# Performance work log

Measured on AMD Instinct MI355X. Metric: run time of the kernel, lower is better.

Reference implementation:

```python
import jax, jax.numpy as jnp
import numpy as np

D_MODEL = 1024
NUM_HEADS = 16
D_FF = 4096
BATCH = 4
SEQ = 1024
EPS = 1e-5
ROPE_THETA = 10000.0


def trunc_normal(key, shape):
    # approximate torch trunc_normal_(mean=0, std=1, a=-2, b=2)
    return jax.random.truncated_normal(key, -2.0, 2.0, shape, dtype=jnp.float32)


def setup_inputs() -> dict:
    key = jax.random.key(0)
    ks = jax.random.split(key, 10)
    d, h, f = D_MODEL, NUM_HEADS, D_FF
    return {
        "x": jax.random.normal(ks[0], (BATCH, SEQ, d), dtype=jnp.float32),
        "wq": trunc_normal(ks[1], (d, d)),
        "wk": trunc_normal(ks[2], (d, d)),
        "wv": trunc_normal(ks[3], (d, d)),
        "wo": trunc_normal(ks[4], (d, d)),
        "w1": trunc_normal(ks[5], (f, d)),
        "w2": trunc_normal(ks[6], (d, f)),
        "w3": trunc_normal(ks[7], (f, d)),
        "g1": trunc_normal(ks[8], (d,)),
        "g2": trunc_normal(ks[9], (d,)),
    }


def rms_norm(x, g):
    # source sums (x^2 + eps) then divides by d -> mean(x^2) + eps
    rms = jnp.sqrt(jnp.mean(jnp.square(x), axis=-1, keepdims=True) + EPS)
    return x * g / rms


def apply_rope(x, pos):
    # x: [b, h, s, d_k]; interleaved-pair rotation, theta=ROPE_THETA
    dk = x.shape[-1]
    inv_freq = ROPE_THETA ** (-jnp.arange(0, dk, 2, dtype=jnp.float32) / dk)
    ang = pos[:, None].astype(jnp.float32) * inv_freq[None, :]  # [s, dk/2]
    cos, sin = jnp.cos(ang), jnp.sin(ang)
    x1, x2 = x[..., 0::2], x[..., 1::2]
    r1 = x1 * cos - x2 * sin
    r2 = x1 * sin + x2 * cos
    return jnp.stack([r1, r2], axis=-1).reshape(x.shape)


def reference(x, wq, wk, wv, wo, w1, w2, w3, g1, g2):
    b, s, d = x.shape
    h, dk = NUM_HEADS, d // NUM_HEADS
    pos = jnp.arange(s)

    # --- attention sub-block (pre-norm) ---
    y = rms_norm(x, g1)
    q = (y @ wq.T).reshape(b, s, h, dk).transpose(0, 2, 1, 3)
    k = (y @ wk.T).reshape(b, s, h, dk).transpose(0, 2, 1, 3)
    v = (y @ wv.T).reshape(b, s, h, dk).transpose(0, 2, 1, 3)
    q = apply_rope(q, pos)
    k = apply_rope(k, pos)
    scores = jnp.einsum('bhqd,bhkd->bhqk', q, k) / jnp.sqrt(jnp.float32(dk))
    causal = jnp.tril(jnp.ones((s, s), dtype=bool))
    scores = jnp.where(causal, scores, -jnp.inf)
    attn = jax.nn.softmax(scores, axis=-1)
    ctx = jnp.einsum('bhqk,bhkd->bhqd', attn, v)
    ctx = ctx.transpose(0, 2, 1, 3).reshape(b, s, d)
    x = x + ctx @ wo.T

    # --- SwiGLU FFN sub-block (pre-norm) ---
    y = rms_norm(x, g2)
    l1 = y @ w1.T
    glu = (jax.nn.sigmoid(l1) * l1) * (y @ w3.T)
    return x + glu @ w2.T
```

## Files before the change

### kernel.cpp

```cpp
#include <hip/hip_runtime.h>

typedef __bf16 bf16;
typedef __attribute__((ext_vector_type(8))) __bf16 bf16x8;
typedef __attribute__((ext_vector_type(4))) float f32x4;

static __device__ __forceinline__ int swz4(int r) { return (r & 3) ^ ((r >> 2) & 3); }

static __device__ __forceinline__ void async_cp16(void* lds, const void* g) {
  __builtin_amdgcn_global_load_lds((__attribute__((address_space(1))) void*)g,
                                   (__attribute__((address_space(3))) void*)lds,
                                   16, 0, 0);
}

static __device__ __forceinline__ f32x4 mfma16(bf16x8 a, bf16x8 b, f32x4 c) {
  return __builtin_amdgcn_mfma_f32_16x16x32_bf16(a, b, c, 0, 0, 0);
}

static __device__ __forceinline__ unsigned short bfbits(float f) {
  bf16 b = (bf16)f;
  return __builtin_bit_cast(unsigned short, b);
}

extern "C" __global__ void prep_kernel(
    const float* __restrict__ wq, const float* __restrict__ wk,
    const float* __restrict__ wv, const float* __restrict__ wo,
    const float* __restrict__ w1, const float* __restrict__ w3,
    const float* __restrict__ w2,
    unsigned short* __restrict__ WQH, unsigned short* __restrict__ WQL,
    unsigned short* __restrict__ WKH, unsigned short* __restrict__ WKL,
    unsigned short* __restrict__ WVH, unsigned short* __restrict__ WOH,
    unsigned short* __restrict__ W1H, unsigned short* __restrict__ W3H,
    unsigned short* __restrict__ W2H, float2* __restrict__ rope) {
  const int seg = blockIdx.y;
  const int i = blockIdx.x * 256 + threadIdx.x;
  if (seg == 7) {
    if (i >= 32768) return;
    int s = i >> 5, fi = i & 31;
    float inv_freq = powf(10000.0f, -(2.0f * (float)fi) / 64.0f);
    float ang = (float)s * inv_freq;
    float2 cs;
    cs.x = cosf(ang);
    cs.y = sinf(ang);
    rope[i] = cs;
    return;
  }
  const float* src;
  unsigned short* hi_;
  unsigned short* lo_ = nullptr;
  int n4;
  switch (seg) {
    case 0: src = wq; hi_ = WQH; lo_ = WQL; n4 = 262144; break;
    case 1: src = wk; hi_ = WKH; lo_ = WKL; n4 = 262144; break;
    case 2: src = wv; hi_ = WVH; n4 = 262144; break;
    case 3: src = wo; hi_ = WOH; n4 = 262144; break;
    case 4: src = w1; hi_ = W1H; n4 = 1048576; break;
    case 5: src = w3; hi_ = W3H; n4 = 1048576; break;
    default: src = w2; hi_ = W2H; n4 = 1048576; break;
  }
  if (i >= n4) return;
  float4 v = ((const float4*)src)[i];
  bf16 b0 = (bf16)v.x, b1 = (bf16)v.y, b2 = (bf16)v.z, b3 = (bf16)v.w;
  ushort4 oh;
  oh.x = __builtin_bit_cast(unsigned short, b0);
  oh.y = __builtin_bit_cast(unsigned short, b1);
  oh.z = __builtin_bit_cast(unsigned short, b2);
  oh.w = __builtin_bit_cast(unsigned short, b3);
  ((ushort4*)hi_)[i] = oh;
  if (lo_) {
    ushort4 ol;
    ol.x = bfbits(v.x - (float)b0);
    ol.y = bfbits(v.y - (float)b1);
    ol.z = bfbits(v.z - (float)b2);
    ol.w = bfbits(v.w - (float)b3);
    ((ushort4*)lo_)[i] = ol;
  }
}

extern "C" __global__ __launch_bounds__(256) void rmsnorm_kernel(
    const float* __restrict__ x, const float* __restrict__ g,
    unsigned short* __restrict__ yhi, unsigned short* __restrict__ ylo) {
  int row = blockIdx.x;
  int t = threadIdx.x;
  const float4 xv = *(const float4*)(x + (size_t)row * 1024 + t * 4);
  float ss = xv.x * xv.x + xv.y * xv.y + xv.z * xv.z + xv.w * xv.w;
#pragma unroll
  for (int d = 1; d < 64; d <<= 1) ss += __shfl_xor(ss, d, 64);
  __shared__ float red[4];
  if ((t & 63) == 0) red[t >> 6] = ss;
  __syncthreads();
  float tot = red[0] + red[1] + red[2] + red[3];
  float inv = 1.0f / sqrtf(tot * (1.0f / 1024.0f) + 1e-5f);
  const float4 gv = *(const float4*)(g + t * 4);
  float y0 = xv.x * gv.x * inv, y1 = xv.y * gv.y * inv;
  float y2 = xv.z * gv.z * inv, y3 = xv.w * gv.w * inv;
  bf16 b0 = (bf16)y0, b1 = (bf16)y1, b2 = (bf16)y2, b3 = (bf16)y3;
  ushort4 oh;
  oh.x = __builtin_bit_cast(unsigned short, b0);
  oh.y = __builtin_bit_cast(unsigned short, b1);
  oh.z = __builtin_bit_cast(unsigned short, b2);
  oh.w = __builtin_bit_cast(unsigned short, b3);
  ((ushort4*)yhi)[(size_t)row * 256 + t] = oh;
  if (ylo) {
    ushort4 ol;
    ol.x = bfbits(y0 - (float)b0);
    ol.y = bfbits(y1 - (float)b1);
    ol.z = bfbits(y2 - (float)b2);
    ol.w = bfbits(y3 - (float)b3);
    ((ushort4*)ylo)[(size_t)row * 256 + t] = ol;
  }
}

template <int EPI>
__global__ __launch_bounds__(256, 2) void gemm_nt(
    const bf16* __restrict__ A, const bf16* __restrict__ B, int M, int N, int K, int ldk,
    float* __restrict__ outF, bf16* __restrict__ outB,
    const float* __restrict__ resF) {
  A += (size_t)blockIdx.z * K;
  B += (size_t)blockIdx.z * K;
  __shared__ alignas(16) bf16 As[128 * 32];
  __shared__ alignas(16) bf16 Bs[128 * 32];
  const int tid = threadIdx.x;
  const int lane = tid & 63, wave = tid >> 6;
  const int lo = lane & 15, hi = lane >> 4;
  const int wm = wave >> 1, wn = wave & 1;
  const size_t tm = (size_t)blockIdx.y * 128, tn = (size_t)blockIdx.x * 128;
  f32x4 acc[4][4] = {};
  for (int k0 = 0; k0 < K; k0 += 32) {
    __syncthreads();
#pragma unroll
    for (int i2 = 0; i2 < 2; i2++) {
      int p = tid + 256 * i2;
      int row = p >> 2, kcp = p & 3;
      int kcl = kcp ^ swz4(row);
      async_cp16((char*)As + (size_t)p * 16, A + (tm + row) * (size_t)ldk + k0 + kcl * 8);
      async_cp16((char*)Bs + (size_t)p * 16, B + (tn + row) * (size_t)ldk + k0 + kcl * 8);
    }
    __syncthreads();
    bf16x8 fa[4], fb[4];
#pragma unroll
    for (int i = 0; i < 4; i++) {
      int ra = wm * 64 + i * 16 + lo;
      fa[i] = *(const bf16x8*)((const char*)As + ra * 64 + ((hi ^ swz4(ra)) << 4));
      int rb = wn * 64 + i * 16 + lo;
      fb[i] = *(const bf16x8*)((const char*)Bs + rb * 64 + ((hi ^ swz4(rb)) << 4));
    }
    __builtin_amdgcn_s_setprio(1);
#pragma unroll
    for (int i = 0; i < 4; i++)
#pragma unroll
      for (int j = 0; j < 4; j++) acc[i][j] = mfma16(fa[i], fb[j], acc[i][j]);
    __builtin_amdgcn_s_setprio(0);
  }
#pragma unroll
  for (int i = 0; i < 4; i++)
#pragma unroll
    for (int j = 0; j < 4; j++)
#pragma unroll
      for (int r = 0; r < 4; r++) {
        size_t m = tm + wm * 64 + i * 16 + hi * 4 + r;
        size_t n = tn + wn * 64 + j * 16 + lo;
        float v = acc[i][j][r];
        if constexpr (EPI == 0) {
          size_t idx = (((m >> 10) * 16 + (n >> 6)) * 64 + (n & 63)) * 1024 + (m & 1023);
          outB[idx] = (bf16)v;
        } else if constexpr (EPI == 1) {
          size_t idx = m * (size_t)N + n;
          outF[idx] = v + resF[idx];
        } else {
          atomicAdd(&outF[m * (size_t)N + n], v);
        }
      }
}

extern "C" __global__ __launch_bounds__(512, 2) void gemm_up_kernel(
    const bf16* __restrict__ A, const bf16* __restrict__ B1,
    const bf16* __restrict__ B3, bf16* __restrict__ G) {
  __shared__ alignas(16) bf16 LA[2][2][256][32];
  __shared__ alignas(16) bf16 LB1[2][2][128][32];
  __shared__ alignas(16) bf16 LB3[2][2][128][32];
  const int tid = threadIdx.x;
  const int lane = tid & 63, wave = tid >> 6;
  const int lo = lane & 15, hi = lane >> 4;
  const int wm = wave >> 1, wn = wave & 1;
  const size_t tm = (size_t)blockIdx.y * 256, tn = (size_t)blockIdx.x * 128;

  f32x4 acc1[4][4] = {}, acc3[4][4] = {};

  auto stageA = [&](int kt, int kh, int buf) {
#pragma unroll
    for (int i2 = 0; i2 < 2; i2++) {
      int s = i2 * 512 + tid;
      int r = s >> 2, c = s & 3;
      async_cp16((char*)&LA[buf][kh][0][0] + (size_t)s * 16,
                 A + (tm + r) * (size_t)1024 + kt * 64 + kh * 32 + ((c ^ (r & 3)) << 3));
    }
  };
  auto stageB = [&](const bf16* __restrict__ Bsrc, bf16* dstBase, int kt, int kh) {
    int r = tid >> 2, c = tid & 3;
    async_cp16((char*)dstBase + (size_t)tid * 16,
               Bsrc + (tn + r) * (size_t)1024 + kt * 64 + kh * 32 + ((c ^ (r & 3)) << 3));
  };

  stageA(0, 0, 0);
  stageB(B1, &LB1[0][0][0][0], 0, 0);
  stageB(B3, &LB3[0][0][0][0], 0, 0);
  stageA(0, 1, 0);
  stageB(B1, &LB1[0][1][0][0], 0, 1);
  stageB(B3, &LB3[0][1][0][0], 0, 1);
  stageA(1, 0, 1);
  stageB(B1, &LB1[1][0][0][0], 1, 0);
  stageB(B3, &LB3[1][0][0][0], 1, 0);
  asm volatile("s_waitcnt vmcnt(4)");
  __builtin_amdgcn_s_barrier();

  for (int t = 0; t < 16; t++) {
    const int p = t & 1;
    bf16x8 fa[4], fb[4];
#pragma unroll
    for (int i = 0; i < 4; i++) {
      int ra = wm * 64 + i * 16 + lo;
      fa[i] = *(const bf16x8*)&LA[p][0][ra][(hi ^ (ra & 3)) << 3];
      int rb = wn * 64 + i * 16 + lo;
      fb[i] = *(const bf16x8*)&LB1[p][0][rb][(hi ^ (rb & 3)) << 3];
    }
    if (t + 1 < 16) stageA(t + 1, 1, p ^ 1);
    __builtin_amdgcn_s_barrier();
    asm volatile("s_waitcnt lgkmcnt(0)");
    __builtin_amdgcn_sched_barrier(0);
    __builtin_amdgcn_s_setprio(1);
#pragma unroll
    for (int i = 0; i < 4; i++)
#pragma unroll
      for (int j = 0; j < 4; j++) acc1[i][j] = mfma16(fa[i], fb[j], acc1[i][j]);
    __builtin_amdgcn_s_setprio(0);
    __builtin_amdgcn_s_barrier();
#pragma unroll
    for (int i = 0; i < 4; i++) {
      int rb = wn * 64 + i * 16 + lo;
      fb[i] = *(const bf16x8*)&LB3[p][0][rb][(hi ^ (rb & 3)) << 3];
    }
    if (t + 1 < 16) {
      stageB(B1, &LB1[p ^ 1][1][0][0], t + 1, 1);
      stageB(B3, &LB3[p ^ 1][1][0][0], t + 1, 1);
    }
    __builtin_amdgcn_s_barrier();
    asm volatile("s_waitcnt lgkmcnt(0)");
    __builtin_amdgcn_sched_barrier(0);
    __builtin_amdgcn_s_setprio(1);
#pragma unroll
    for (int i = 0; i < 4; i++)
#pragma unroll
      for (int j = 0; j < 4; j++) acc3[i][j] = mfma16(fa[i], fb[j], acc3[i][j]);
    __builtin_amdgcn_s_setprio(0);
    __builtin_amdgcn_s_barrier();
#pragma unroll
    for (int i = 0; i < 4; i++) {
      int ra = wm * 64 + i * 16 + lo;
      fa[i] = *(const bf16x8*)&LA[p][1][ra][(hi ^ (ra & 3)) << 3];
      int rb = wn * 64 + i * 16 + lo;
      fb[i] = *(const bf16x8*)&LB1[p][1][rb][(hi ^ (rb & 3)) << 3];
    }
    if (t + 2 < 16) stageA(t + 2, 0, p);
    __builtin_amdgcn_s_barrier();
    asm volatile("s_waitcnt lgkmcnt(0)");
    __builtin_amdgcn_sched_barrier(0);
    __builtin_amdgcn_s_setprio(1);
#pragma unroll
    for (int i = 0; i < 4; i++)
#pragma unroll
      for (int j = 0; j < 4; j++) acc1[i][j] = mfma16(fa[i], fb[j], acc1[i][j]);
    __builtin_amdgcn_s_setprio(0);
    __builtin_amdgcn_s_barrier();
#pragma unroll
    for (int i = 0; i < 4; i++) {
      int rb = wn * 64 + i * 16 + lo;
      fb[i] = *(const bf16x8*)&LB3[p][1][rb][(hi ^ (rb & 3)) << 3];
    }
    if (t + 2 < 16) {
      stageB(B1, &LB1[p][0][0][0], t + 2, 0);
      stageB(B3, &LB3[p][0][0][0], t + 2, 0);
    }
    __builtin_amdgcn_s_barrier();
    asm volatile("s_waitcnt lgkmcnt(0)");
    __builtin_amdgcn_sched_barrier(0);
    __builtin_amdgcn_s_setprio(1);
#pragma unroll
    for (int i = 0; i < 4; i++)
#pragma unroll
      for (int j = 0; j < 4; j++) acc3[i][j] = mfma16(fa[i], fb[j], acc3[i][j]);
    __builtin_amdgcn_s_setprio(0);
    if (t + 2 < 16) {
      asm volatile("s_waitcnt vmcnt(4)");
    } else if (t + 1 < 16) {
      asm volatile("s_waitcnt vmcnt(0)");
    }
    __builtin_amdgcn_s_barrier();
  }

#pragma unroll
  for (int i = 0; i < 4; i++)
#pragma unroll
    for (int j = 0; j < 4; j++)
#pragma unroll
      for (int r = 0; r < 4; r++) {
        size_t m = tm + wm * 64 + i * 16 + hi * 4 + r;
        size_t n = tn + wn * 64 + j * 16 + lo;
        float v1 = acc1[i][j][r], v3 = acc3[i][j][r];
        G[m * 4096 + n] = (bf16)(v1 / (1.0f + __expf(-v1)) * v3);
      }
}

extern "C" __global__ __launch_bounds__(256, 2) void gemm_qk_kernel(
    const bf16* __restrict__ Ah, const bf16* __restrict__ Al,
    const bf16* __restrict__ BhQ, const bf16* __restrict__ BlQ,
    const bf16* __restrict__ BhK, const bf16* __restrict__ BlK,
    const float2* __restrict__ rope,
    bf16* __restrict__ OhQ, bf16* __restrict__ OlQ,
    bf16* __restrict__ OhK, bf16* __restrict__ OlK) {
  const bf16* Bh = blockIdx.z ? BhK : BhQ;
  const bf16* Bl = blockIdx.z ? BlK : BlQ;
  bf16* Oh = blockIdx.z ? OhK : OhQ;
  bf16* Ol = blockIdx.z ? OlK : OlQ;
  __shared__ alignas(16) bf16 Ahs[128 * 32], Als[128 * 32], Bhs[128 * 32], Bls[128 * 32];
  const int tid = threadIdx.x;
  const int lane = tid & 63, wave = tid >> 6;
  const int lo = lane & 15, hi = lane >> 4;
  const int wm = wave >> 1, wn = wave & 1;
  const size_t tm = (size_t)blockIdx.y * 128, tn = (size_t)blockIdx.x * 128;
  const int K = 1024;
  f32x4 acc[4][4] = {};
  for (int k0 = 0; k0 < K; k0 += 32) {
    __syncthreads();
#pragma unroll
    for (int i2 = 0; i2 < 2; i2++) {
      int p = tid + 256 * i2;
      int row = p >> 2;
      int kcl = (p & 3) ^ swz4(row);
      size_t ga = (tm + row) * (size_t)K + k0 + kcl * 8;
      size_t gb = (tn + row) * (size_t)K + k0 + kcl * 8;
      async_cp16((char*)Ahs + (size_t)p * 16, Ah + ga);
      async_cp16((char*)Als + (size_t)p * 16, Al + ga);
      async_cp16((char*)Bhs + (size_t)p * 16, Bh + gb);
      async_cp16((char*)Bls + (size_t)p * 16, Bl + gb);
    }
    __syncthreads();
    bf16x8 fah[4], fal[4], fbh[4], fbl[4];
#pragma unroll
    for (int i = 0; i < 4; i++) {
      int ra = wm * 64 + i * 16 + lo;
      int oa = ra * 64 + ((hi ^ swz4(ra)) << 4);
      fah[i] = *(const bf16x8*)((const char*)Ahs + oa);
      fal[i] = *(const bf16x8*)((const char*)Als + oa);
      int rb = wn * 64 + i * 16 + lo;
      int ob = rb * 64 + ((hi ^ swz4(rb)) << 4);
      fbh[i] = *(const bf16x8*)((const char*)Bhs + ob);
      fbl[i] = *(const bf16x8*)((const char*)Bls + ob);
    }
    __builtin_amdgcn_s_setprio(1);
#pragma unroll
    for (int i = 0; i < 4; i++)
#pragma unroll
      for (int j = 0; j < 4; j++) {
        f32x4 a = acc[i][j];
        a = mfma16(fah[i], fbh[j], a);
        a = mfma16(fah[i], fbl[j], a);
        a = mfma16(fal[i], fbh[j], a);
        acc[i][j] = a;
      }
    __builtin_amdgcn_s_setprio(0);
  }
#pragma unroll
  for (int i = 0; i < 4; i++)
#pragma unroll
    for (int j = 0; j < 4; j++)
#pragma unroll
      for (int r = 0; r < 4; r++) {
        float v = acc[i][j][r];
        float vp = __shfl_xor(v, 1, 64);
        size_t m = tm + wm * 64 + i * 16 + hi * 4 + r;
        size_t n = tn + wn * 64 + j * 16 + lo;
        int s = (int)(m & 1023);
        int pi = (int)((n & 63) >> 1);
        float2 cs = rope[s * 32 + pi];
        float res = (n & 1) ? (vp * cs.y + v * cs.x) : (v * cs.x - vp * cs.y);
        size_t idx = (((m >> 10) * 16 + (n >> 6)) * 1024 + (m & 1023)) * 64 + (n & 63);
        bf16 hb = (bf16)res;
        Oh[idx] = hb;
        Ol[idx] = (bf16)(res - (float)hb);
      }
}

extern "C" __global__ __launch_bounds__(256, 4) void flash_kernel(
    const bf16* __restrict__ qhi, const bf16* __restrict__ qlo,
    const bf16* __restrict__ khi, const bf16* __restrict__ klo,
    const bf16* __restrict__ vT, bf16* __restrict__ ctx) {
  const int bid = blockIdx.x;
  const int qb = bid >> 6;
  const int bh = bid & 63;
  const int tid = threadIdx.x;
  const int wave = tid >> 6, lane = tid & 63;
  const int lo = lane & 15, hi = lane >> 4;

  __shared__ alignas(16) bf16 Ksh[2][64][32];
  __shared__ alignas(16) bf16 Ksl[2][64][32];
  __shared__ alignas(16) bf16 Vs[2][64][32];
  __shared__ alignas(16) bf16 P[4][16][72];

  size_t qoff = ((size_t)bh * 1024 + qb * 64 + wave * 16 + lo) * 64;
  bf16x8 qh[2], ql[2];
#pragma unroll
  for (int ks = 0; ks < 2; ks++) {
    qh[ks] = *(const bf16x8*)(qhi + qoff + ks * 32 + hi * 8);
    ql[ks] = *(const bf16x8*)(qlo + qoff + ks * 32 + hi * 8);
  }

  const int srow = tid >> 2;
  const int scl = (tid & 3) ^ swz4(srow);
  const size_t kgb = (size_t)bh * 1024 * 64;
  const size_t vgb = ((size_t)bh * 64 + srow) * 1024;

  float mrun[4] = {-1e30f, -1e30f, -1e30f, -1e30f};
  float lrun[4] = {0.f, 0.f, 0.f, 0.f};
  f32x4 o[4] = {};
  const float scale = 0.125f;

  for (int kt = 0; kt <= qb; kt++) {
    __syncthreads();
#pragma unroll
    for (int i = 0; i < 2; i++) {
      int p = tid + 256 * i;
      size_t gk = kgb + (size_t)(kt * 64 + srow) * 64 + i * 32 + scl * 8;
      async_cp16((char*)Ksh + (size_t)p * 16, khi + gk);
      async_cp16((char*)Ksl + (size_t)p * 16, klo + gk);
      async_cp16((char*)Vs + (size_t)p * 16, vT + vgb + kt * 64 + i * 32 + scl * 8);
    }
    __syncthreads();

    f32x4 sv[4];
    __builtin_amdgcn_s_setprio(1);
#pragma unroll
    for (int nb = 0; nb < 4; nb++) {
      f32x4 a = {0.f, 0.f, 0.f, 0.f};
#pragma unroll
      for (int ks = 0; ks < 2; ks++) {
        int row = nb * 16 + lo;
        int off16 = (ks * 64 + row) * 4 + (hi ^ swz4(row));
        bf16x8 kh = *(const bf16x8*)((const char*)Ksh + off16 * 16);
        bf16x8 kl = *(const bf16x8*)((const char*)Ksl + off16 * 16);
        a = mfma16(qh[ks], kh, a);
        a = mfma16(qh[ks], kl, a);
        a = mfma16(ql[ks], kh, a);
      }
      sv[nb] = a;
    }
    __builtin_amdgcn_s_setprio(0);

    const bool mt = (kt == qb);
#pragma unroll
    for (int nb = 0; nb < 4; nb++)
#pragma unroll
      for (int r = 0; r < 4; r++) {
        float s = sv[nb][r] * scale;
        if (mt) {
          int kp = nb * 16 + lo;
          int qr = wave * 16 + hi * 4 + r;
          if (kp > qr) s = -1e30f;
        }
        sv[nb][r] = s;
      }
    float mnew[4], rs[4];
#pragma unroll
    for (int r = 0; r < 4; r++) {
      float mx = fmaxf(fmaxf(sv[0][r], sv[1][r]), fmaxf(sv[2][r], sv[3][r]));
#pragma unroll
      for (int d = 1; d < 16; d <<= 1) mx = fmaxf(mx, __shfl_xor(mx, d, 64));
      mnew[r] = fmaxf(mrun[r], mx);
      float sc = __expf(mrun[r] - mnew[r]);
      lrun[r] *= sc;
#pragma unroll
      for (int db = 0; db < 4; db++) o[db][r] *= sc;
      mrun[r] = mnew[r];
      rs[r] = 0.f;
    }
#pragma unroll
    for (int nb = 0; nb < 4; nb++)
#pragma unroll
      for (int r = 0; r < 4; r++) {
        float p = __expf(sv[nb][r] - mnew[r]);
        bf16 pb = (bf16)p;
        rs[r] += (float)pb;
        P[wave][hi * 4 + r][nb * 16 + lo] = pb;
      }
#pragma unroll
    for (int r = 0; r < 4; r++) {
      float t = rs[r];
#pragma unroll
      for (int d = 1; d < 16; d <<= 1) t += __shfl_xor(t, d, 64);
      lrun[r] += t;
    }
    bf16x8 pa[2];
#pragma unroll
    for (int ks = 0; ks < 2; ks++) pa[ks] = *(const bf16x8*)&P[wave][lo][ks * 32 + hi * 8];
    __builtin_amdgcn_s_setprio(1);
#pragma unroll
    for (int db = 0; db < 4; db++)
#pragma unroll
      for (int ks = 0; ks < 2; ks++) {
        int row = db * 16 + lo;
        int off16 = (ks * 64 + row) * 4 + (hi ^ swz4(row));
        bf16x8 vf = *(const bf16x8*)((const char*)Vs + off16 * 16);
        o[db] = mfma16(pa[ks], vf, o[db]);
      }
    __builtin_amdgcn_s_setprio(0);
  }
  int b = bh >> 4, h = bh & 15;
#pragma unroll
  for (int db = 0; db < 4; db++)
#pragma unroll
    for (int r = 0; r < 4; r++) {
      float val = o[db][r] / lrun[r];
      size_t row = (size_t)b * 1024 + qb * 64 + wave * 16 + hi * 4 + r;
      ctx[row * 1024 + h * 64 + db * 16 + lo] = (bf16)val;
    }
}


extern "C" void kernel_launch(void* const* d_in, const int* in_sizes, int n_in,
                              void* d_out, int out_size, void* d_ws, size_t ws_size,
                              hipStream_t stream) {
  (void)in_sizes; (void)n_in; (void)out_size; (void)ws_size;
  const float* x  = (const float*)d_in[0];
  const float* wq = (const float*)d_in[1];
  const float* wk = (const float*)d_in[2];
  const float* wv = (const float*)d_in[3];
  const float* wo = (const float*)d_in[4];
  const float* w1 = (const float*)d_in[5];
  const float* w2 = (const float*)d_in[6];
  const float* w3 = (const float*)d_in[7];
  const float* g1 = (const float*)d_in[8];
  const float* g2 = (const float*)d_in[9];
  float* out = (float*)d_out;

  char* ws = (char*)d_ws;
  size_t off = 0;
  auto alloc = [&](size_t bytes) {
    char* p = ws + off;
    off += (bytes + 255) & ~(size_t)255;
    return p;
  };
  const size_t MB2 = 1024u * 1024u * 2u;
  const size_t MB8 = 4096u * 1024u * 2u;
  void* WQH = alloc(MB2);  void* WQL = alloc(MB2);
  void* WKH = alloc(MB2);  void* WKL = alloc(MB2);
  void* WVH = alloc(MB2);  void* WOH = alloc(MB2);
  void* W1H = alloc(MB8);  void* W3H = alloc(MB8);  void* W2H = alloc(MB8);
  void* ROPE = alloc(32768u * 8u);
  void* Y1H = alloc(MB8);  void* Y1L = alloc(MB8);
  void* QH = alloc(MB8);   void* QL = alloc(MB8);
  void* KH = alloc(MB8);   void* KL = alloc(MB8);
  void* VT = alloc(MB8);
  void* CTX = alloc(MB8);
  void* Y2H = alloc(MB8);
  void* GLU = QH;

  prep_kernel<<<dim3(4096, 8), dim3(256), 0, stream>>>(
      wq, wk, wv, wo, w1, w3, w2,
      (unsigned short*)WQH, (unsigned short*)WQL, (unsigned short*)WKH,
      (unsigned short*)WKL, (unsigned short*)WVH, (unsigned short*)WOH,
      (unsigned short*)W1H, (unsigned short*)W3H, (unsigned short*)W2H,
      (float2*)ROPE);

  rmsnorm_kernel<<<dim3(4096), dim3(256), 0, stream>>>(
      x, g1, (unsigned short*)Y1H, (unsigned short*)Y1L);

  gemm_qk_kernel<<<dim3(8, 32, 2), dim3(256), 0, stream>>>(
      (const bf16*)Y1H, (const bf16*)Y1L,
      (const bf16*)WQH, (const bf16*)WQL, (const bf16*)WKH, (const bf16*)WKL,
      (const float2*)ROPE,
      (bf16*)QH, (bf16*)QL, (bf16*)KH, (bf16*)KL);

  gemm_nt<0><<<dim3(8, 32), dim3(256), 0, stream>>>(
      (const bf16*)Y1H, (const bf16*)WVH, 4096, 1024, 1024, 1024,
      nullptr, (bf16*)VT, nullptr);

  flash_kernel<<<dim3(1024), dim3(256), 0, stream>>>(
      (const bf16*)QH, (const bf16*)QL, (const bf16*)KH, (const bf16*)KL,
      (const bf16*)VT, (bf16*)CTX);

  gemm_nt<1><<<dim3(8, 32), dim3(256), 0, stream>>>(
      (const bf16*)CTX, (const bf16*)WOH, 4096, 1024, 1024, 1024,
      out, nullptr, x);

  rmsnorm_kernel<<<dim3(4096), dim3(256), 0, stream>>>(
      out, g2, (unsigned short*)Y2H, nullptr);

  gemm_up_kernel<<<dim3(32, 16), dim3(512), 0, stream>>>(
      (const bf16*)Y2H, (const bf16*)W1H, (const bf16*)W3H, (bf16*)GLU);

  gemm_nt<5><<<dim3(8, 32, 4), dim3(256), 0, stream>>>(
      (const bf16*)GLU, (const bf16*)W2H, 4096, 1024, 1024, 4096,
      out, nullptr, nullptr);
}
```

Before: 346.6 us.

## Remap GEMM block indices per XCD and change LDS swizzle pattern

Replaces the 2D/3D grids of every GEMM kernel with a 1D grid whose block index is decoded so that consecutive blocks landing on the same XCD (bid & 7) share M-rows or N-columns. The aim is better L2 reuse within each XCD on the chiplet-based MI355X. It also changes the LDS swizzle function to (r>>1)&3 and applies it in gemm_up, which targets different bank-conflict behavior for the 16-byte fragment reads. The new swizzle must stay consistent between the async copy writes and the fragment reads; both sides are updated.

```diff
diff --git a/kernel.cpp b/kernel.cpp
--- a/kernel.cpp
+++ b/kernel.cpp
@@ -4,7 +4,7 @@
 typedef __attribute__((ext_vector_type(8))) __bf16 bf16x8;
 typedef __attribute__((ext_vector_type(4))) float f32x4;
 
-static __device__ __forceinline__ int swz4(int r) { return (r & 3) ^ ((r >> 2) & 3); }
+static __device__ __forceinline__ int swz4(int r) { return (r >> 1) & 3; }
 
 static __device__ __forceinline__ void async_cp16(void* lds, const void* g) {
   __builtin_amdgcn_global_load_lds((__attribute__((address_space(1))) void*)g,
@@ -112,18 +112,23 @@
 
 template <int EPI>
 __global__ __launch_bounds__(256, 2) void gemm_nt(
-    const bf16* __restrict__ A, const bf16* __restrict__ B, int M, int N, int K, int ldk,
+    const bf16* __restrict__ A, const bf16* __restrict__ B, int N, int K, int ldk,
     float* __restrict__ outF, bf16* __restrict__ outB,
     const float* __restrict__ resF) {
-  A += (size_t)blockIdx.z * K;
-  B += (size_t)blockIdx.z * K;
+  const int bid = blockIdx.x;
+  const int xcd = bid & 7, sq = bid >> 3;
+  const int z = sq >> 5;
+  const int rem = sq & 31;
+  const size_t tm = (size_t)(xcd * 4 + (rem >> 3)) * 128;
+  const size_t tn = (size_t)(rem & 7) * 128;
+  A += (size_t)z * K;
+  B += (size_t)z * K;
   __shared__ alignas(16) bf16 As[128 * 32];
   __shared__ alignas(16) bf16 Bs[128 * 32];
   const int tid = threadIdx.x;
   const int lane = tid & 63, wave = tid >> 6;
   const int lo = lane & 15, hi = lane >> 4;
   const int wm = wave >> 1, wn = wave & 1;
-  const size_t tm = (size_t)blockIdx.y * 128, tn = (size_t)blockIdx.x * 128;
   f32x4 acc[4][4] = {};
   for (int k0 = 0; k0 < K; k0 += 32) {
     __syncthreads();
@@ -182,7 +187,10 @@
   const int lane = tid & 63, wave = tid >> 6;
   const int lo = lane & 15, hi = lane >> 4;
   const int wm = wave >> 1, wn = wave & 1;
-  const size_t tm = (size_t)blockIdx.y * 256, tn = (size_t)blockIdx.x * 128;
+  const int bid = blockIdx.x;
+  const int xcd = bid & 7, sq = bid >> 3;
+  const size_t tn = (size_t)(xcd * 4 + (sq & 3)) * 128;
+  const size_t tm = (size_t)(sq >> 2) * 256;
 
   f32x4 acc1[4][4] = {}, acc3[4][4] = {};
 
@@ -192,13 +200,13 @@
       int s = i2 * 512 + tid;
       int r = s >> 2, c = s & 3;
       async_cp16((char*)&LA[buf][kh][0][0] + (size_t)s * 16,
-                 A + (tm + r) * (size_t)1024 + kt * 64 + kh * 32 + ((c ^ (r & 3)) << 3));
+                 A + (tm + r) * (size_t)1024 + kt * 64 + kh * 32 + ((c ^ swz4(r)) << 3));
     }
   };
   auto stageB = [&](const bf16* __restrict__ Bsrc, bf16* dstBase, int kt, int kh) {
     int r = tid >> 2, c = tid & 3;
     async_cp16((char*)dstBase + (size_t)tid * 16,
-               Bsrc + (tn + r) * (size_t)1024 + kt * 64 + kh * 32 + ((c ^ (r & 3)) << 3));
+               Bsrc + (tn + r) * (size_t)1024 + kt * 64 + kh * 32 + ((c ^ swz4(r)) << 3));
   };
 
   stageA(0, 0, 0);
@@ -219,9 +227,9 @@
 #pragma unroll
     for (int i = 0; i < 4; i++) {
       int ra = wm * 64 + i * 16 + lo;
-      fa[i] = *(const bf16x8*)&LA[p][0][ra][(hi ^ (ra & 3)) << 3];
+      fa[i] = *(const bf16x8*)&LA[p][0][ra][(hi ^ swz4(ra)) << 3];
       int rb = wn * 64 + i * 16 + lo;
-      fb[i] = *(const bf16x8*)&LB1[p][0][rb][(hi ^ (rb & 3)) << 3];
+      fb[i] = *(const bf16x8*)&LB1[p][0][rb][(hi ^ swz4(rb)) << 3];
     }
     if (t + 1 < 16) stageA(t + 1, 1, p ^ 1);
     __builtin_amdgcn_s_barrier();
@@ -237,7 +245,7 @@
 #pragma unroll
     for (int i = 0; i < 4; i++) {
       int rb = wn * 64 + i * 16 + lo;
-      fb[i] = *(const bf16x8*)&LB3[p][0][rb][(hi ^ (rb & 3)) << 3];
+      fb[i] = *(const bf16x8*)&LB3[p][0][rb][(hi ^ swz4(rb)) << 3];
     }
     if (t + 1 < 16) {
       stageB(B1, &LB1[p ^ 1][1][0][0], t + 1, 1);
@@ -256,9 +264,9 @@
 #pragma unroll
     for (int i = 0; i < 4; i++) {
       int ra = wm * 64 + i * 16 + lo;
-      fa[i] = *(const bf16x8*)&LA[p][1][ra][(hi ^ (ra & 3)) << 3];
+      fa[i] = *(const bf16x8*)&LA[p][1][ra][(hi ^ swz4(ra)) << 3];
       int rb = wn * 64 + i * 16 + lo;
-      fb[i] = *(const bf16x8*)&LB1[p][1][rb][(hi ^ (rb & 3)) << 3];
+      fb[i] = *(const bf16x8*)&LB1[p][1][rb][(hi ^ swz4(rb)) << 3];
     }
     if (t + 2 < 16) stageA(t + 2, 0, p);
     __builtin_amdgcn_s_barrier();
@@ -274,7 +282,7 @@
 #pragma unroll
     for (int i = 0; i < 4; i++) {
       int rb = wn * 64 + i * 16 + lo;
-      fb[i] = *(const bf16x8*)&LB3[p][1][rb][(hi ^ (rb & 3)) << 3];
+      fb[i] = *(const bf16x8*)&LB3[p][1][rb][(hi ^ swz4(rb)) << 3];
     }
     if (t + 2 < 16) {
       stageB(B1, &LB1[p][0][0][0], t + 2, 0);
@@ -317,16 +325,21 @@
     const float2* __restrict__ rope,
     bf16* __restrict__ OhQ, bf16* __restrict__ OlQ,
     bf16* __restrict__ OhK, bf16* __restrict__ OlK) {
-  const bf16* Bh = blockIdx.z ? BhK : BhQ;
-  const bf16* Bl = blockIdx.z ? BlK : BlQ;
-  bf16* Oh = blockIdx.z ? OhK : OhQ;
-  bf16* Ol = blockIdx.z ? OlK : OlQ;
+  const int bid = blockIdx.x;
+  const int xcd = bid & 7, sq = bid >> 3;
+  const int zqk = sq >> 5;
+  const int rem = sq & 31;
+  const size_t tm = (size_t)(xcd * 4 + (rem >> 3)) * 128;
+  const size_t tn = (size_t)(rem & 7) * 128;
+  const bf16* Bh = zqk ? BhK : BhQ;
+  const bf16* Bl = zqk ? BlK : BlQ;
+  bf16* Oh = zqk ? OhK : OhQ;
+  bf16* Ol = zqk ? OlK : OlQ;
   __shared__ alignas(16) bf16 Ahs[128 * 32], Als[128 * 32], Bhs[128 * 32], Bls[128 * 32];
   const int tid = threadIdx.x;
   const int lane = tid & 63, wave = tid >> 6;
   const int lo = lane & 15, hi = lane >> 4;
   const int wm = wave >> 1, wn = wave & 1;
-  const size_t tm = (size_t)blockIdx.y * 128, tn = (size_t)blockIdx.x * 128;
   const int K = 1024;
   f32x4 acc[4][4] = {};
   for (int k0 = 0; k0 < K; k0 += 32) {
@@ -573,31 +586,31 @@
   rmsnorm_kernel<<<dim3(4096), dim3(256), 0, stream>>>(
       x, g1, (unsigned short*)Y1H, (unsigned short*)Y1L);
 
-  gemm_qk_kernel<<<dim3(8, 32, 2), dim3(256), 0, stream>>>(
+  gemm_qk_kernel<<<dim3(512), dim3(256), 0, stream>>>(
       (const bf16*)Y1H, (const bf16*)Y1L,
       (const bf16*)WQH, (const bf16*)WQL, (const bf16*)WKH, (const bf16*)WKL,
       (const float2*)ROPE,
       (bf16*)QH, (bf16*)QL, (bf16*)KH, (bf16*)KL);
 
-  gemm_nt<0><<<dim3(8, 32), dim3(256), 0, stream>>>(
-      (const bf16*)Y1H, (const bf16*)WVH, 4096, 1024, 1024, 1024,
+  gemm_nt<0><<<dim3(256), dim3(256), 0, stream>>>(
+      (const bf16*)Y1H, (const bf16*)WVH, 1024, 1024, 1024,
       nullptr, (bf16*)VT, nullptr);
 
   flash_kernel<<<dim3(1024), dim3(256), 0, stream>>>(
       (const bf16*)QH, (const bf16*)QL, (const bf16*)KH, (const bf16*)KL,
       (const bf16*)VT, (bf16*)CTX);
 
-  gemm_nt<1><<<dim3(8, 32), dim3(256), 0, stream>>>(
-      (const bf16*)CTX, (const bf16*)WOH, 4096, 1024, 1024, 1024,
+  gemm_nt<1><<<dim3(256), dim3(256), 0, stream>>>(
+      (const bf16*)CTX, (const bf16*)WOH, 1024, 1024, 1024,
       out, nullptr, x);
 
   rmsnorm_kernel<<<dim3(4096), dim3(256), 0, stream>>>(
       out, g2, (unsigned short*)Y2H, nullptr);
 
-  gemm_up_kernel<<<dim3(32, 16), dim3(512), 0, stream>>>(
+  gemm_up_kernel<<<dim3(512), dim3(512), 0, stream>>>(
       (const bf16*)Y2H, (const bf16*)W1H, (const bf16*)W3H, (bf16*)GLU);
 
-  gemm_nt<5><<<dim3(8, 32, 4), dim3(256), 0, stream>>>(
-      (const bf16*)GLU, (const bf16*)W2H, 4096, 1024, 1024, 4096,
+  gemm_nt<5><<<dim3(1024), dim3(256), 0, stream>>>(
+      (const bf16*)GLU, (const bf16*)W2H, 1024, 1024, 4096,
       out, nullptr, nullptr);
 }
```

Measured after the change: 330.6 us. 4.6% less time.
